# Performance work log

Measured on AMD Instinct MI355X. Metric: run time of the kernel, lower is better.

## Reference

```python
import jax, jax.numpy as jnp
import numpy as np

NMS_PRE, NMS_POST, NMS_THRESH = 1024, 512, 0.7
B, A, FEAT = 4, 70400, 27648
BN_EPS = 1e-5


def _bev_iou(boxes):
    # boxes: [K, 7] (x, y, z, dx, dy, dz, ry); axis-aligned BEV IoU
    x, y, dx, dy = boxes[:, 0], boxes[:, 1], boxes[:, 3], boxes[:, 4]
    x1, x2 = x - 0.5 * dx, x + 0.5 * dx
    y1, y2 = y - 0.5 * dy, y + 0.5 * dy
    iw = jnp.clip(jnp.minimum(x2[:, None], x2[None, :]) - jnp.maximum(x1[:, None], x1[None, :]), 0.0)
    ih = jnp.clip(jnp.minimum(y2[:, None], y2[None, :]) - jnp.maximum(y1[:, None], y1[None, :]), 0.0)
    inter = iw * ih
    area = dx * dy
    return inter / jnp.clip(area[:, None] + area[None, :] - inter, 1e-6)


def _greedy_nms(boxes, thresh):
    # boxes sorted by score desc; returns keep mask [K]
    K = boxes.shape[0]
    iou = _bev_iou(boxes)
    idx = jnp.arange(K)

    def step(keep, i):
        sup = (iou[i] > thresh) & (idx > i) & keep[i]
        return keep & ~sup, None

    keep, _ = jax.lax.scan(step, jnp.ones(K, dtype=bool), jnp.arange(K))
    return keep


def _proposal_one(box, cls):
    # box: [A, 7], cls: [A, n_cls]  ->  padded rois [NPOST,7], scores [NPOST], labels [NPOST]
    score = jnp.max(cls, axis=-1)
    label = jnp.argmax(cls, axis=-1)
    top_score, top_idx = jax.lax.top_k(score, NMS_PRE)
    top_box = box[top_idx]
    keep = _greedy_nms(top_box, NMS_THRESH)
    # stable: kept entries first, preserving score order
    order = jnp.argsort(jnp.where(keep, jnp.arange(NMS_PRE), NMS_PRE + jnp.arange(NMS_PRE)))
    sel = order[:NMS_POST]
    valid = jnp.arange(NMS_POST) < jnp.minimum(jnp.sum(keep), NMS_POST)
    rois = jnp.where(valid[:, None], top_box[sel], 0.0)
    roi_score = jnp.where(valid, top_score[sel], 0.0)
    roi_label = jnp.where(valid, label[top_idx][sel], 0) + 1  # +1 as in module
    return rois, roi_score, roi_label


def _bn_relu(h, g, b):
    # eval-mode BN with running_mean=0, running_var=1
    return jax.nn.relu(h * (g / jnp.sqrt(1.0 + BN_EPS)) + b)


def _decode(reg, anchors):
    # ResidualCoder_v1.decode_torch
    xa, ya, za = anchors[..., 0], anchors[..., 1], anchors[..., 2]
    dxa, dya, dza, ra = anchors[..., 3], anchors[..., 4], anchors[..., 5], anchors[..., 6]
    xt, yt, zt = reg[..., 0], reg[..., 1], reg[..., 2]
    dxt, dyt, dzt, rt = reg[..., 3], reg[..., 4], reg[..., 5], reg[..., 6]
    diag = jnp.sqrt(dxa * dxa + dya * dya)
    return jnp.stack([
        xt * diag + xa, yt * diag + ya, zt * dza + za,
        jnp.exp(dxt) * dxa, jnp.exp(dyt) * dya, jnp.exp(dzt) * dza,
        rt + ra], axis=-1)


def _rotate_z(box, ang):
    # rotate x,y of box [..., 7] by ang [...]
    c, s = jnp.cos(ang), jnp.sin(ang)
    x = box[..., 0] * c - box[..., 1] * s
    y = box[..., 0] * s + box[..., 1] * c
    return jnp.concatenate([x[..., None], y[..., None], box[..., 2:]], axis=-1)


def reference(rpn_box_preds, rpn_cls_preds, pooled_features,
              Ws1, g1, b1, Ws2, g2, b2,
              Wc1, gc1, bc1, Wc2, gc2, bc2, Wc3, bc3,
              Wr1, gr1, br1, Wr2, gr2, br2, Wr3, br3):
    # proposal_layer: per-batch topk + NMS + padded scatter (vmapped)
    rois, roi_scores, roi_labels = jax.vmap(_proposal_one)(rpn_box_preds, rpn_cls_preds)

    # shared / cls / reg heads (1x1 Conv1d == per-roi MLP), dropout off (eval)
    x = _bn_relu(pooled_features @ Ws1.T, g1, b1)
    x = _bn_relu(x @ Ws2.T, g2, b2)
    c = _bn_relu(x @ Wc1.T, gc1, bc1)
    c = _bn_relu(c @ Wc2.T, gc2, bc2)
    cls_preds = c @ Wc3.T + bc3          # [B*NPOST, 1]
    r = _bn_relu(x @ Wr1.T, gr1, br1)
    r = _bn_relu(r @ Wr2.T, gr2, br2)
    reg_preds = r @ Wr3.T + br3          # [B*NPOST, 7]

    bsz = rois.shape[0]
    cls_preds = cls_preds.reshape(bsz, -1, cls_preds.shape[-1])
    reg_preds = reg_preds.reshape(bsz, -1, 7)

    # generate_predict_box: decode against detached rois with xyz zeroed
    anchors = jax.lax.stop_gradient(rois)
    anchors = anchors.at[..., 0:3].set(0.0)
    box_ct = _decode(reg_preds, anchors)
    box_preds = _rotate_z(box_ct, rois[..., 6])
    box_preds = jnp.concatenate([box_preds[..., 0:3] + rois[..., 0:3], box_preds[..., 3:]], axis=-1)

    return jnp.concatenate([cls_preds, box_preds, roi_scores[..., None]], axis=-1)  # [B, NPOST, 9]


def setup_inputs():
    key = jax.random.key(0)
    ks = jax.random.split(key, 32)
    u = jax.random.uniform(ks[0], (B, A, 7), dtype=jnp.float32)
    lo = jnp.array([0.0, -40.0, -2.0, 1.5, 1.4, 1.0, -3.14159], jnp.float32)
    hi = jnp.array([70.0, 40.0, 0.0, 4.5, 2.0, 2.0, 3.14159], jnp.float32)
    rpn_box_preds = lo + u * (hi - lo)
    rpn_cls_preds = jax.random.normal(ks[1], (B, A, 3), dtype=jnp.float32)
    pooled_features = jax.random.normal(ks[2], (B * NMS_POST, FEAT), dtype=jnp.float32) * 0.1

    def w(k, o, i, std=None):
        s = (1.0 / np.sqrt(i)) if std is None else std
        return jax.random.normal(k, (o, i), dtype=jnp.float32) * s

    d = dict(
        rpn_box_preds=rpn_box_preds, rpn_cls_preds=rpn_cls_preds, pooled_features=pooled_features,
        Ws1=w(ks[3], 256, FEAT), g1=jnp.ones(256), b1=jnp.zeros(256),
        Ws2=w(ks[4], 256, 256), g2=jnp.ones(256), b2=jnp.zeros(256),
        Wc1=w(ks[5], 256, 256), gc1=jnp.ones(256), bc1=jnp.zeros(256),
        Wc2=w(ks[6], 256, 256), gc2=jnp.ones(256), bc2=jnp.zeros(256),
        Wc3=w(ks[7], 1, 256), bc3=jnp.zeros(1),
        Wr1=w(ks[8], 256, 256), gr1=jnp.ones(256), br1=jnp.zeros(256),
        Wr2=w(ks[9], 256, 256), gr2=jnp.ones(256), br2=jnp.zeros(256),
        Wr3=w(ks[10], 7, 256, std=0.001), br3=jnp.zeros(7),
    )
    return d
```

## Files before the change

### kernel.cpp

```cpp
#include <hip/hip_runtime.h>
#include <cstdint>

typedef unsigned int u32;
typedef unsigned long long u64;
typedef unsigned short u16;

#define BATCH 4
#define A_CNT 70400
#define FEAT 27648
#define KSPLIT 12
#define KCHUNK 2304
#define NTILE_IT 36

typedef __attribute__((ext_vector_type(8))) short bf16x8;
typedef __attribute__((ext_vector_type(4))) float f32x4;
typedef __attribute__((ext_vector_type(2))) u32 u32x2;
typedef __attribute__((ext_vector_type(4))) u32 u32x4;

constexpr size_t OF_KEYS = 0;
constexpr size_t OF_TBOX = OF_KEYS + 1126400;
constexpr size_t OF_TSC  = OF_TBOX + 114688;
constexpr size_t OF_BX1  = OF_TSC + 16384;
constexpr size_t OF_BX2  = OF_BX1 + 16384;
constexpr size_t OF_BY1  = OF_BX2 + 16384;
constexpr size_t OF_BY2  = OF_BY1 + 16384;
constexpr size_t OF_BAR  = OF_BY2 + 16384;
constexpr size_t OF_MASK = OF_BAR + 16384;
constexpr size_t OF_ROIS = OF_MASK + 524288;
constexpr size_t OF_RSC  = OF_ROIS + 57344;
constexpr size_t OF_BSW  = OF_RSC + 8192;
constexpr size_t OF_PART = OF_BSW + 14155776;
constexpr size_t WS_NEED = OF_PART + 33554432;

__device__ __forceinline__ u32 keyOf(float f) {
  u32 u = __float_as_uint(f);
  return (u & 0x80000000u) ? ~u : (u | 0x80000000u);
}
__device__ __forceinline__ float keyToF(u32 k) {
  u32 u = (k & 0x80000000u) ? (k ^ 0x80000000u) : ~k;
  return __uint_as_float(u);
}
__device__ __forceinline__ u16 f2bf(float f) {
  u32 u = __float_as_uint(f);
  u32 r = 0x7FFFu + ((u >> 16) & 1u);
  return (u16)((u + r) >> 16);
}
__device__ __forceinline__ void gload_lds16(const void* g, void* l) {
  auto gp = reinterpret_cast<const __attribute__((address_space(1))) unsigned int*>(
      reinterpret_cast<uintptr_t>(g));
  auto lp = reinterpret_cast<__attribute__((address_space(3))) unsigned int*>(
      reinterpret_cast<uintptr_t>(l));
  __builtin_amdgcn_global_load_lds(gp, lp, 16, 0, 0);
}
__device__ __forceinline__ u64 shflx64(u64 v, int m) {
  u32 lo = (u32)v, hi = (u32)(v >> 32);
  lo = __shfl_xor(lo, m, 64);
  hi = __shfl_xor(hi, m, 64);
  return ((u64)hi << 32) | lo;
}
__device__ __forceinline__ u32x4 pack8(float4 a, float4 b) {
  u32x4 o;
  o.x = (u32)f2bf(a.x) | ((u32)f2bf(a.y) << 16);
  o.y = (u32)f2bf(a.z) | ((u32)f2bf(a.w) << 16);
  o.z = (u32)f2bf(b.x) | ((u32)f2bf(b.y) << 16);
  o.w = (u32)f2bf(b.z) | ((u32)f2bf(b.w) << 16);
  return o;
}

__global__ __launch_bounds__(1024) void k_fatA(const float* __restrict__ cls,
    const float* __restrict__ Ws1, u32* __restrict__ keys, u32* __restrict__ Bsw)
{
  int bid = blockIdx.x;
  int t = threadIdx.x;
  if (bid < 864) {
    u32 w = (u32)bid * 1024u + t;
    u32 tile = w >> 11;
    u32 rem = w & 2047u;
    u32 n = rem >> 3;
    u32 pq = (rem & 7u) << 4;
    u32 q0 = pq ^ ((n & 7u) << 4);
    u32 col0 = tile * 64u + (q0 >> 1);
    const float* src = Ws1 + (size_t)n * FEAT + col0;
    float4 f0 = *(const float4*)src;
    float4 f1 = *(const float4*)(src + 4);
    ((u32x4*)Bsw)[w] = pack8(f0, f1);
    return;
  }
  u32 g = (u32)(bid - 864) * 1024u + t;
  float s0 = cls[(size_t)g * 3 + 0];
  float s1 = cls[(size_t)g * 3 + 1];
  float s2 = cls[(size_t)g * 3 + 2];
  keys[g] = keyOf(fmaxf(s0, fmaxf(s1, s2)));
}

__global__ __launch_bounds__(1024) void k_big(const u32* __restrict__ keys,
    const float* __restrict__ boxes, const float* __restrict__ A,
    const u32* __restrict__ Bsw, float* __restrict__ part,
    float* __restrict__ tbox, float* __restrict__ tsc,
    float* __restrict__ bx1, float* __restrict__ bx2, float* __restrict__ by1,
    float* __restrict__ by2, float* __restrict__ bar)
{
  __shared__ __align__(16) char smem[131072];
  int bid = blockIdx.x;
  int t = threadIdx.x;
  if (bid < 4) {
    int b = bid;
    int lane = t & 63, wv = t >> 6;
    const u32* kb = keys + (size_t)b * A_CNT;
    u64* s = (u64*)smem;
    u32* partials = (u32*)(smem + 16384);
    u32* ccp = (u32*)(smem + 16448);
    u32 h[35];
#pragma unroll
    for (int j = 0; j < 35; ++j) {
      int g0 = t + ((2 * j) << 10);
      int g1 = t + ((2 * j + 1) << 10);
      u32 a = (g0 < A_CNT) ? (kb[g0] >> 16) : 0u;
      u32 c2 = (g1 < A_CNT) ? (kb[g1] >> 16) : 0u;
      h[j] = a | (c2 << 16);
    }
    if (t == 0) ccp[0] = 0u;
    u32 lo = 0, hi = 65536;
    while (hi - lo > 1) {
      u32 mid = (lo + hi) >> 1;
      u32 c = 0;
#pragma unroll
      for (int j = 0; j < 35; ++j) {
        c += ((h[j] & 0xFFFFu) >= mid) ? 1u : 0u;
        c += ((h[j] >> 16) >= mid) ? 1u : 0u;
      }
#pragma unroll
      for (int o = 32; o > 0; o >>= 1) c += __shfl_xor(c, o, 64);
      __syncthreads();
      if (lane == 0) partials[wv] = c;
      __syncthreads();
      u32 tot = 0;
#pragma unroll
      for (int w2 = 0; w2 < 16; ++w2) tot += partials[w2];
      if (tot >= 1024u) lo = mid; else hi = mid;
    }
    u32 kth = lo;
    __syncthreads();
    u32 kc = kb[t];
#pragma unroll 1
    for (int i = 0; i < 69; ++i) {
      int g = t + (i << 10);
      u32 k = kc;
      if (i < 68) {
        int gn = t + ((i + 1) << 10);
        kc = (gn < A_CNT) ? kb[gn] : 0u;
      }
      bool pass = (g < A_CNT) && ((k >> 16) >= kth);
      u64 mm = __ballot(pass);
      if (mm) {
        int leader = __ffsll((unsigned long long)mm) - 1;
        u32 base = 0;
        if (lane == leader) base = atomicAdd(ccp, (u32)__popcll(mm));
        base = __shfl(base, leader, 64);
        if (pass) {
          u32 pos = base + (u32)__popcll(mm & ((1ull << lane) - 1ull));
          if (pos < 2048u) s[pos] = ((u64)k << 32) | (u32)(~(u32)g);
        }
      }
    }
    __syncthreads();
    u32 m = ccp[0]; if (m > 2048u) m = 2048u;
    for (int e = t; e < 2048; e += 1024) if (e >= (int)m) s[e] = 0ull;
    __syncthreads();
    {
      u64 v0 = s[2 * t], v1 = s[2 * t + 1];
#pragma unroll
      for (u32 k = 2; k <= 128; k <<= 1) {
        bool desc = ((t & (k >> 1)) == 0);
#pragma unroll
        for (u32 j = (k >> 1); j >= 2; j >>= 1) {
          u32 mmk = j >> 1;
          u64 p0 = shflx64(v0, mmk);
          u64 p1 = shflx64(v1, mmk);
          bool up = ((t & mmk) == 0);
          bool mx = (desc == up);
          v0 = mx ? (v0 > p0 ? v0 : p0) : (v0 < p0 ? v0 : p0);
          v1 = mx ? (v1 > p1 ? v1 : p1) : (v1 < p1 ? v1 : p1);
        }
        if (desc ? (v0 < v1) : (v0 > v1)) { u64 tmp = v0; v0 = v1; v1 = tmp; }
      }
      s[2 * t] = v0; s[2 * t + 1] = v1;
      __syncthreads();
      for (u32 k = 256; k <= 2048; k <<= 1) {
        for (u32 j = k >> 1; j >= 128; j >>= 1) {
          for (int e = t; e < 2048; e += 1024) {
            u32 p = (u32)e ^ j;
            if (p > (u32)e) {
              bool d2 = ((e & k) == 0);
              u64 x = s[e], y = s[p];
              if (d2 ? (x < y) : (x > y)) { s[e] = y; s[p] = x; }
            }
          }
          __syncthreads();
        }
        u64 v0 = s[2 * t], v1 = s[2 * t + 1];
        bool desc = ((t & (k >> 1)) == 0);
#pragma unroll
        for (u32 j = 64; j >= 2; j >>= 1) {
          u32 mmk = j >> 1;
          u64 p0 = shflx64(v0, mmk);
          u64 p1 = shflx64(v1, mmk);
          bool up = ((t & mmk) == 0);
          bool mx = (desc == up);
          v0 = mx ? (v0 > p0 ? v0 : p0) : (v0 < p0 ? v0 : p0);
          v1 = mx ? (v1 > p1 ? v1 : p1) : (v1 < p1 ? v1 : p1);
        }
        if (desc ? (v0 < v1) : (v0 > v1)) { u64 tmp = v0; v0 = v1; v1 = tmp; }
        s[2 * t] = v0; s[2 * t + 1] = v1;
        __syncthreads();
      }
    }
    u64 comp = s[t];
    u32 kk = (u32)(comp >> 32);
    u32 a = ~(u32)(comp & 0xFFFFFFFFull);
    int o = b * 1024 + t;
    tsc[o] = keyToF(kk);
    const float* bp = boxes + ((size_t)b * A_CNT + a) * 7;
    float x = bp[0], y = bp[1], z = bp[2], dx = bp[3], dy = bp[4], dz = bp[5], rr = bp[6];
    float* tb = tbox + (size_t)o * 7;
    tb[0] = x; tb[1] = y; tb[2] = z; tb[3] = dx; tb[4] = dy; tb[5] = dz; tb[6] = rr;
    {
#pragma clang fp contract(off)
      bx1[o] = x - 0.5f * dx; bx2[o] = x + 0.5f * dx;
      by1[o] = y - 0.5f * dy; by2[o] = y + 0.5f * dy;
      bar[o] = dx * dy;
    }
    return;
  }
  int bid2 = bid - 4;
  int ks = bid2 >> 4;
  int mt = bid2 & 15;
  int lane = t & 63, wvid = t >> 6;
  int row16 = lane & 15, kgrp = lane >> 4;
  int gm = wvid >> 2, gn = wvid & 3;

  f32x4 acc[2][4];
#pragma unroll
  for (int i = 0; i < 2; ++i)
#pragma unroll
    for (int j = 0; j < 4; ++j) acc[i][j] = (f32x4){0.f, 0.f, 0.f, 0.f};

  int arow = t >> 3;
  const float* ap_base = A + ((size_t)(mt * 128 + arow)) * FEAT + (size_t)ks * KCHUNK + (t & 7) * 8;
  int asw = (arow & 7) << 4;
  int awoff = arow * 128 + (((t & 7) * 16) ^ asw);
  const char* bsrc_base = (const char*)Bsw + ((size_t)(ks * NTILE_IT)) * 32768 + wvid * 2048 + lane * 16;
  int bdoff = wvid * 2048 + lane * 16;
  char* Abase = smem;
  char* Bbase = smem + 32768;

  int aoff[2][2], boff[4][2];
#pragma unroll
  for (int ksub = 0; ksub < 2; ++ksub) {
    int qq = ksub * 64 + kgrp * 16;
#pragma unroll
    for (int mf = 0; mf < 2; ++mf) {
      int row = gm * 32 + mf * 16 + row16;
      aoff[mf][ksub] = row * 128 + (qq ^ ((row & 7) << 4));
    }
#pragma unroll
    for (int nf = 0; nf < 4; ++nf) {
      int n = gn * 64 + nf * 16 + row16;
      boff[nf][ksub] = n * 128 + (qq ^ ((n & 7) << 4));
    }
  }

  float4 gaold0, gaold1;
  {
    const float4* ap0 = (const float4*)ap_base;
    float4 a00 = ap0[0], a01 = ap0[1];
    gload_lds16(bsrc_base, Bbase + bdoff);
    gload_lds16(bsrc_base + 1024, Bbase + bdoff + 1024);
    const float4* ap1 = (const float4*)(ap_base + 64);
    gaold0 = ap1[0]; gaold1 = ap1[1];
    const char* bs1 = bsrc_base + 32768;
    gload_lds16(bs1, Bbase + 32768 + bdoff);
    gload_lds16(bs1 + 1024, Bbase + 32768 + bdoff + 1024);
    *(u32x4*)(Abase + awoff) = pack8(a00, a01);
    asm volatile("s_waitcnt lgkmcnt(0)" ::: "memory");
    asm volatile("s_waitcnt vmcnt(4)" ::: "memory");
    __builtin_amdgcn_sched_barrier(0);
    __builtin_amdgcn_s_barrier();
  }

#pragma unroll 1
  for (int it = 0; it < NTILE_IT; ++it) {
    char* Acur = Abase + ((it & 1) << 14);
    char* Bcur = Bbase + (it % 3) * 32768;
    bool pf = (it + 2 < NTILE_IT);
    float4 gn0, gn1;
    if (pf) {
      const float4* ap = (const float4*)(ap_base + (it + 2) * 64);
      gn0 = ap[0]; gn1 = ap[1];
      const char* bs = bsrc_base + (size_t)(it + 2) * 32768;
      char* Bn = Bbase + ((it + 2) % 3) * 32768;
      gload_lds16(bs, Bn + bdoff);
      gload_lds16(bs + 1024, Bn + bdoff + 1024);
    }
    bf16x8 af[2][2], bf[4][2];
#pragma unroll
    for (int ksub = 0; ksub < 2; ++ksub) {
#pragma unroll
      for (int mf = 0; mf < 2; ++mf) af[mf][ksub] = *(const bf16x8*)(Acur + aoff[mf][ksub]);
#pragma unroll
      for (int nf = 0; nf < 4; ++nf) bf[nf][ksub] = *(const bf16x8*)(Bcur + boff[nf][ksub]);
    }
#pragma unroll
    for (int ksub = 0; ksub < 2; ++ksub)
#pragma unroll
      for (int mf = 0; mf < 2; ++mf)
#pragma unroll
        for (int nf = 0; nf < 4; ++nf)
          acc[mf][nf] = __builtin_amdgcn_mfma_f32_16x16x32_bf16(af[mf][ksub], bf[nf][ksub], acc[mf][nf], 0, 0, 0);
    if (it + 1 < NTILE_IT) {
      char* An = Abase + (((it + 1) & 1) << 14);
      *(u32x4*)(An + awoff) = pack8(gaold0, gaold1);
      gaold0 = gn0; gaold1 = gn1;
      asm volatile("s_waitcnt lgkmcnt(0)" ::: "memory");
      if (pf) asm volatile("s_waitcnt vmcnt(4)" ::: "memory");
      else    asm volatile("s_waitcnt vmcnt(0)" ::: "memory");
      __builtin_amdgcn_sched_barrier(0);
      __builtin_amdgcn_s_barrier();
    }
  }
  float* pb = part + (size_t)ks * 524288;
#pragma unroll
  for (int mf = 0; mf < 2; ++mf) {
    int orow = mt * 128 + gm * 32 + mf * 16 + kgrp * 4;
#pragma unroll
    for (int nf = 0; nf < 4; ++nf) {
      int col = gn * 64 + nf * 16 + row16;
#pragma unroll
      for (int rr = 0; rr < 4; ++rr)
        pb[(size_t)(orow + rr) * 256 + col] = acc[mf][nf][rr];
    }
  }
}

__global__ __launch_bounds__(1024) void k_mask(const float* __restrict__ bx1,
    const float* __restrict__ bx2, const float* __restrict__ by1,
    const float* __restrict__ by2, const float* __restrict__ bar,
    u32* __restrict__ mask)
{
  __shared__ float csm[16][5][64];
  int tt = threadIdx.x;
  int ug = tt >> 6, ln = tt & 63;
  int unit = blockIdx.x * 16 + ug;
  int b = unit >> 8, cbk = (unit >> 4) & 15, rb = unit & 15;
  int o = b * 1024, jc0 = cbk * 64;
  int r = rb * 64 + ln;
  csm[ug][0][ln] = bx1[o + jc0 + ln];
  csm[ug][1][ln] = bx2[o + jc0 + ln];
  csm[ug][2][ln] = by1[o + jc0 + ln];
  csm[ug][3][ln] = by2[o + jc0 + ln];
  csm[ug][4][ln] = bar[o + jc0 + ln];
  __syncthreads();
  float rx1 = bx1[o + r], rx2 = bx2[o + r], ry1 = by1[o + r], ry2 = by2[o + r], rar = bar[o + r];
  u32 w0 = 0, w1 = 0;
  {
#pragma clang fp contract(off)
    for (int c = 0; c < 64; ++c) {
      int jc = jc0 + c;
      float iw = fminf(rx2, csm[ug][1][c]) - fmaxf(rx1, csm[ug][0][c]); iw = fmaxf(iw, 0.0f);
      float ih = fminf(ry2, csm[ug][3][c]) - fmaxf(ry1, csm[ug][2][c]); ih = fmaxf(ih, 0.0f);
      float inter = iw * ih;
      float den = fmaxf(rar + csm[ug][4][c] - inter, 1e-6f);
      float iou = inter / den;
      if ((iou > 0.7f) && (jc > r)) {
        if (c < 32) w0 |= 1u << c; else w1 |= 1u << (c - 32);
      }
    }
  }
  mask[((size_t)(o + r)) * 32 + cbk * 2 + 0] = w0;
  mask[((size_t)(o + r)) * 32 + cbk * 2 + 1] = w1;
}

#define CHUNK_STEP(CUR, NXT, C) do {                                            \
    if ((C) + 1 < 32) {                                                         \
      int nb = ((C) + 1) * 1024 + el;                                           \
      _Pragma("unroll")                                                         \
      for (int i = 0; i < 32; ++i) NXT[i] = M[(size_t)(nb + i * 32)];           \
    }                                                                           \
    u32 w = R;                                                                  \
    _Pragma("unroll")                                                           \
    for (int i = 0; i < 32; ++i) w |= ((w >> i) & 1u) ? 0u : CUR[i];            \
    u32 wfin = __shfl(w, (C), 64);                                              \
    u32 m0 = 0, m1 = 0, m2 = 0, m3 = 0;                                         \
    _Pragma("unroll")                                                           \
    for (int i = 0; i < 32; i += 4) {                                           \
      m0 |= ((wfin >> (i + 0)) & 1u) ? 0u : CUR[i + 0];                         \
      m1 |= ((wfin >> (i + 1)) & 1u) ? 0u : CUR[i + 1];                         \
      m2 |= ((wfin >> (i + 2)) & 1u) ? 0u : CUR[i + 2];                         \
      m3 |= ((wfin >> (i + 3)) & 1u) ? 0u : CUR[i + 3];                         \
    }                                                                           \
    R |= (m0 | m1) | (m2 | m3);                                                 \
  } while (0)

__global__ __launch_bounds__(64) void k_nms(const u32* __restrict__ mask,
    const float* __restrict__ tbox, const float* __restrict__ tsc,
    float* __restrict__ rois, float* __restrict__ rsc)
{
  int b = blockIdx.x;
  int lane = threadIdx.x;
  int el = lane & 31;
  const u32* M = mask + (size_t)b * 1024 * 32;
  u32 R = 0;
  u32 bufA[32], bufB[32];
#pragma unroll
  for (int i = 0; i < 32; ++i) bufA[i] = M[(size_t)(i * 32 + el)];
#pragma unroll 1
  for (int c = 0; c < 32; c += 2) {
    CHUNK_STEP(bufA, bufB, c);
    CHUNK_STEP(bufB, bufA, c + 1);
  }
  u32 keepw = (lane < 32) ? ~R : 0u;
  int c = __popc(keepw);
  int pre = c;
  for (int d = 1; d < 64; d <<= 1) {
    int v = __shfl_up(pre, d, 64);
    if (lane >= d) pre += v;
  }
  int total = __shfl(pre, 31, 64);
  int base = pre - c;
  if (lane < 32) {
    u32 w = keepw;
    int rank = base;
    while (w) {
      int bit = __ffs(w) - 1;
      w &= w - 1;
      if (rank < 512) {
        int r = lane * 32 + bit;
        const float* tb = tbox + ((size_t)b * 1024 + r) * 7;
        float* rp = rois + ((size_t)b * 512 + rank) * 7;
        rp[0] = tb[0]; rp[1] = tb[1]; rp[2] = tb[2]; rp[3] = tb[3];
        rp[4] = tb[4]; rp[5] = tb[5]; rp[6] = tb[6];
        rsc[b * 512 + rank] = tsc[b * 1024 + r];
      }
      rank++;
    }
  }
  for (int z = total + lane; z < 512; z += 64) {
    float* rp = rois + ((size_t)b * 512 + z) * 7;
    rp[0] = rp[1] = rp[2] = rp[3] = rp[4] = rp[5] = rp[6] = 0.0f;
    rsc[b * 512 + z] = 0.0f;
  }
}

__device__ __forceinline__ void layer4(const float (*IN)[256], const float* __restrict__ W,
    const float* __restrict__ g, const float* __restrict__ bb, float (*OUT)[256], int t, int h)
{
  float acc[4] = {0, 0, 0, 0};
  const float* Wrow = W + (size_t)t * 256;
  for (int k = 0; k < 256; k += 4) {
    float4 w4 = *(const float4*)&Wrow[k];
#pragma unroll
    for (int r = 0; r < 4; ++r) {
      float4 xv = *(const float4*)&IN[h * 4 + r][k];
      acc[r] = fmaf(xv.x, w4.x, acc[r]);
      acc[r] = fmaf(xv.y, w4.y, acc[r]);
      acc[r] = fmaf(xv.z, w4.z, acc[r]);
      acc[r] = fmaf(xv.w, w4.w, acc[r]);
    }
  }
  float sc = g[t] / sqrtf(1.0f + 1e-5f);
  float bv = bb[t];
#pragma unroll
  for (int r = 0; r < 4; ++r)
    OUT[h * 4 + r][t] = fmaxf(fmaf(acc[r], sc, bv), 0.0f);
}

__global__ __launch_bounds__(512) void k_chain(const float* __restrict__ part,
    const float* __restrict__ Ws2, const float* __restrict__ Wc1, const float* __restrict__ Wc2,
    const float* __restrict__ Wr1, const float* __restrict__ Wr2,
    const float* __restrict__ g1, const float* __restrict__ b1,
    const float* __restrict__ g2, const float* __restrict__ b2,
    const float* __restrict__ gc1, const float* __restrict__ bc1,
    const float* __restrict__ gc2, const float* __restrict__ bc2,
    const float* __restrict__ gr1, const float* __restrict__ br1,
    const float* __restrict__ gr2, const float* __restrict__ br2,
    const float* __restrict__ Wc3, const float* __restrict__ bc3,
    const float* __restrict__ Wr3, const float* __restrict__ br3,
    const float* __restrict__ rois, const float* __restrict__ rsc,
    float* __restrict__ out)
{
  int bid = blockIdx.x, tid = threadIdx.x;
  int t = tid & 255, h = tid >> 8;
  __shared__ __align__(16) float bufX[8][256];
  __shared__ __align__(16) float bufY[8][256];
  __shared__ __align__(16) float bufC[8][256];
  __shared__ __align__(16) float bufR[8][256];
  __shared__ float hd[64];
  {
    float sc = g1[t] / sqrtf(1.0f + 1e-5f);
    float bv = b1[t];
#pragma unroll
    for (int r = 0; r < 4; ++r) {
      int row = h * 4 + r;
      float s = 0.f;
#pragma unroll
      for (int ks = 0; ks < KSPLIT; ++ks)
        s += part[(size_t)ks * 524288 + (size_t)(bid * 8 + row) * 256 + t];
      bufX[row][t] = fmaxf(fmaf(s, sc, bv), 0.0f);
    }
  }
  __syncthreads();
  layer4(bufX, Ws2, g2, b2, bufY, t, h);
  __syncthreads();
  layer4(bufY, Wc1, gc1, bc1, bufC, t, h);
  layer4(bufY, Wr1, gr1, br1, bufR, t, h);
  __syncthreads();
  layer4(bufC, Wc2, gc2, bc2, bufX, t, h);
  layer4(bufR, Wr2, gr2, br2, bufY, t, h);
  __syncthreads();
  int wv = tid >> 6, ln = tid & 63;
  for (int task = wv; task < 64; task += 8) {
    float p;
    if (task < 8) {
      float4 yv = *(const float4*)&bufX[task][ln * 4];
      float4 w4 = ((const float4*)Wc3)[ln];
      p = yv.x * w4.x + yv.y * w4.y + yv.z * w4.z + yv.w * w4.w;
    } else {
      int i = task - 8, row = i / 7, j = i % 7;
      float4 yv = *(const float4*)&bufY[row][ln * 4];
      float4 w4 = ((const float4*)(Wr3 + j * 256))[ln];
      p = yv.x * w4.x + yv.y * w4.y + yv.z * w4.z + yv.w * w4.w;
    }
#pragma unroll
    for (int off = 32; off > 0; off >>= 1) p += __shfl_xor(p, off, 64);
    if (ln == 0) hd[task] = p;
  }
  __syncthreads();
  if (tid < 8) {
    int m = bid * 8 + tid;
    float clsv = hd[tid] + bc3[0];
    float rg[7];
#pragma unroll
    for (int j = 0; j < 7; ++j) rg[j] = hd[8 + tid * 7 + j] + br3[j];
    const float* R = rois + (size_t)m * 7;
    float rx = R[0], ry = R[1], rz = R[2], dxa = R[3], dya = R[4], dza = R[5], ra = R[6];
    float diag = sqrtf(dxa * dxa + dya * dya);
    float x = rg[0] * diag, y = rg[1] * diag, z = rg[2] * dza;
    float ex = expf(rg[3]) * dxa, ey = expf(rg[4]) * dya, ez = expf(rg[5]) * dza;
    float hr = rg[6] + ra;
    float cc = cosf(ra), sn = sinf(ra);
    float xr = x * cc - y * sn, yr = x * sn + y * cc;
    float* O = out + (size_t)m * 9;
    O[0] = clsv; O[1] = xr + rx; O[2] = yr + ry; O[3] = z + rz;
    O[4] = ex; O[5] = ey; O[6] = ez; O[7] = hr; O[8] = rsc[m];
  }
}

extern "C" void kernel_launch(void* const* d_in, const int* in_sizes, int n_in,
                              void* d_out, int out_size, void* d_ws, size_t ws_size,
                              hipStream_t stream)
{
  const float* rpn_box = (const float*)d_in[0];
  const float* rpn_cls = (const float*)d_in[1];
  const float* pooled  = (const float*)d_in[2];
  const float* Ws1 = (const float*)d_in[3];
  const float* g1  = (const float*)d_in[4];
  const float* b1  = (const float*)d_in[5];
  const float* Ws2 = (const float*)d_in[6];
  const float* g2  = (const float*)d_in[7];
  const float* b2  = (const float*)d_in[8];
  const float* Wc1 = (const float*)d_in[9];
  const float* gc1 = (const float*)d_in[10];
  const float* bc1 = (const float*)d_in[11];
  const float* Wc2 = (const float*)d_in[12];
  const float* gc2 = (const float*)d_in[13];
  const float* bc2 = (const float*)d_in[14];
  const float* Wc3 = (const float*)d_in[15];
  const float* bc3 = (const float*)d_in[16];
  const float* Wr1 = (const float*)d_in[17];
  const float* gr1 = (const float*)d_in[18];
  const float* br1 = (const float*)d_in[19];
  const float* Wr2 = (const float*)d_in[20];
  const float* gr2 = (const float*)d_in[21];
  const float* br2 = (const float*)d_in[22];
  const float* Wr3 = (const float*)d_in[23];
  const float* br3 = (const float*)d_in[24];

  if (ws_size < WS_NEED) return;

  char* ws = (char*)d_ws;
  u32* keys = (u32*)(ws + OF_KEYS);
  float* tbox = (float*)(ws + OF_TBOX);
  float* tsc  = (float*)(ws + OF_TSC);
  float* bx1 = (float*)(ws + OF_BX1);
  float* bx2 = (float*)(ws + OF_BX2);
  float* by1 = (float*)(ws + OF_BY1);
  float* by2 = (float*)(ws + OF_BY2);
  float* bar = (float*)(ws + OF_BAR);
  u32* mask = (u32*)(ws + OF_MASK);
  float* roisb = (float*)(ws + OF_ROIS);
  float* rscb  = (float*)(ws + OF_RSC);
  u32* Bsw = (u32*)(ws + OF_BSW);
  float* part = (float*)(ws + OF_PART);

  k_fatA<<<1139, 1024, 0, stream>>>(rpn_cls, Ws1, keys, Bsw);
  k_big<<<196, 1024, 0, stream>>>(keys, rpn_box, pooled, Bsw, part,
                                  tbox, tsc, bx1, bx2, by1, by2, bar);
  k_mask<<<64, 1024, 0, stream>>>(bx1, bx2, by1, by2, bar, mask);
  k_nms<<<4, 64, 0, stream>>>(mask, tbox, tsc, roisb, rscb);
  k_chain<<<256, 512, 0, stream>>>(part, Ws2, Wc1, Wc2, Wr1, Wr2,
                                   g1, b1, g2, b2, gc1, bc1, gc2, bc2,
                                   gr1, br1, gr2, br2, Wc3, bc3, Wr3, br3,
                                   roisb, rscb, (float*)d_out);
}
```

Before: 216.6 us.

## Fuse IoU mask computation into NMS kernel using LDS-resident mask

Merges the separate IoU-mask kernel and the greedy NMS scan into one kernel per batch. Each of 1024 threads computes its row's suppression bits across all column blocks and stores them in a swizzled 128KB shared-memory mask. One wave then runs the serial scan from LDS instead of global memory. This removes a launch and a global mask round-trip, but cuts mask-compute parallelism from 64 blocks to 4 and drops the cross-chunk prefetch.

```diff
diff --git a/kernel.cpp b/kernel.cpp
--- a/kernel.cpp
+++ b/kernel.cpp
@@ -342,112 +342,95 @@
   }
 }
 
-__global__ __launch_bounds__(1024) void k_mask(const float* __restrict__ bx1,
+__global__ __launch_bounds__(1024) void k_nms(const float* __restrict__ bx1,
     const float* __restrict__ bx2, const float* __restrict__ by1,
     const float* __restrict__ by2, const float* __restrict__ bar,
-    u32* __restrict__ mask)
-{
-  __shared__ float csm[16][5][64];
-  int tt = threadIdx.x;
-  int ug = tt >> 6, ln = tt & 63;
-  int unit = blockIdx.x * 16 + ug;
-  int b = unit >> 8, cbk = (unit >> 4) & 15, rb = unit & 15;
-  int o = b * 1024, jc0 = cbk * 64;
-  int r = rb * 64 + ln;
-  csm[ug][0][ln] = bx1[o + jc0 + ln];
-  csm[ug][1][ln] = bx2[o + jc0 + ln];
-  csm[ug][2][ln] = by1[o + jc0 + ln];
-  csm[ug][3][ln] = by2[o + jc0 + ln];
-  csm[ug][4][ln] = bar[o + jc0 + ln];
-  __syncthreads();
-  float rx1 = bx1[o + r], rx2 = bx2[o + r], ry1 = by1[o + r], ry2 = by2[o + r], rar = bar[o + r];
-  u32 w0 = 0, w1 = 0;
-  {
-#pragma clang fp contract(off)
-    for (int c = 0; c < 64; ++c) {
-      int jc = jc0 + c;
-      float iw = fminf(rx2, csm[ug][1][c]) - fmaxf(rx1, csm[ug][0][c]); iw = fmaxf(iw, 0.0f);
-      float ih = fminf(ry2, csm[ug][3][c]) - fmaxf(ry1, csm[ug][2][c]); ih = fmaxf(ih, 0.0f);
-      float inter = iw * ih;
-      float den = fmaxf(rar + csm[ug][4][c] - inter, 1e-6f);
-      float iou = inter / den;
-      if ((iou > 0.7f) && (jc > r)) {
-        if (c < 32) w0 |= 1u << c; else w1 |= 1u << (c - 32);
-      }
-    }
-  }
-  mask[((size_t)(o + r)) * 32 + cbk * 2 + 0] = w0;
-  mask[((size_t)(o + r)) * 32 + cbk * 2 + 1] = w1;
-}
-
-#define CHUNK_STEP(CUR, NXT, C) do {                                            \
-    if ((C) + 1 < 32) {                                                         \
-      int nb = ((C) + 1) * 1024 + el;                                           \
-      _Pragma("unroll")                                                         \
-      for (int i = 0; i < 32; ++i) NXT[i] = M[(size_t)(nb + i * 32)];           \
-    }                                                                           \
-    u32 w = R;                                                                  \
-    _Pragma("unroll")                                                           \
-    for (int i = 0; i < 32; ++i) w |= ((w >> i) & 1u) ? 0u : CUR[i];            \
-    u32 wfin = __shfl(w, (C), 64);                                              \
-    u32 m0 = 0, m1 = 0, m2 = 0, m3 = 0;                                         \
-    _Pragma("unroll")                                                           \
-    for (int i = 0; i < 32; i += 4) {                                           \
-      m0 |= ((wfin >> (i + 0)) & 1u) ? 0u : CUR[i + 0];                         \
-      m1 |= ((wfin >> (i + 1)) & 1u) ? 0u : CUR[i + 1];                         \
-      m2 |= ((wfin >> (i + 2)) & 1u) ? 0u : CUR[i + 2];                         \
-      m3 |= ((wfin >> (i + 3)) & 1u) ? 0u : CUR[i + 3];                         \
-    }                                                                           \
-    R |= (m0 | m1) | (m2 | m3);                                                 \
-  } while (0)
-
-__global__ __launch_bounds__(64) void k_nms(const u32* __restrict__ mask,
     const float* __restrict__ tbox, const float* __restrict__ tsc,
     float* __restrict__ rois, float* __restrict__ rsc)
 {
-  int b = blockIdx.x;
-  int lane = threadIdx.x;
-  int el = lane & 31;
-  const u32* M = mask + (size_t)b * 1024 * 32;
-  u32 R = 0;
-  u32 bufA[32], bufB[32];
-#pragma unroll
-  for (int i = 0; i < 32; ++i) bufA[i] = M[(size_t)(i * 32 + el)];
+  __shared__ u32 Ml[1024 * 32];
+  int b = blockIdx.x, t = threadIdx.x;
+  int o = b * 1024;
+  float rx1 = bx1[o + t], rx2 = bx2[o + t], ry1 = by1[o + t], ry2 = by2[o + t], rar = bar[o + t];
 #pragma unroll 1
-  for (int c = 0; c < 32; c += 2) {
-    CHUNK_STEP(bufA, bufB, c);
-    CHUNK_STEP(bufB, bufA, c + 1);
-  }
-  u32 keepw = (lane < 32) ? ~R : 0u;
-  int c = __popc(keepw);
-  int pre = c;
-  for (int d = 1; d < 64; d <<= 1) {
-    int v = __shfl_up(pre, d, 64);
-    if (lane >= d) pre += v;
-  }
-  int total = __shfl(pre, 31, 64);
-  int base = pre - c;
-  if (lane < 32) {
-    u32 w = keepw;
-    int rank = base;
-    while (w) {
-      int bit = __ffs(w) - 1;
-      w &= w - 1;
-      if (rank < 512) {
-        int r = lane * 32 + bit;
-        const float* tb = tbox + ((size_t)b * 1024 + r) * 7;
-        float* rp = rois + ((size_t)b * 512 + rank) * 7;
-        rp[0] = tb[0]; rp[1] = tb[1]; rp[2] = tb[2]; rp[3] = tb[3];
-        rp[4] = tb[4]; rp[5] = tb[5]; rp[6] = tb[6];
-        rsc[b * 512 + rank] = tsc[b * 1024 + r];
-      }
-      rank++;
-    }
-  }
-  for (int z = total + lane; z < 512; z += 64) {
-    float* rp = rois + ((size_t)b * 512 + z) * 7;
-    rp[0] = rp[1] = rp[2] = rp[3] = rp[4] = rp[5] = rp[6] = 0.0f;
-    rsc[b * 512 + z] = 0.0f;
+  for (int cbk = 0; cbk < 16; ++cbk) {
+    int jc0 = cbk * 64;
+    u32 w0 = 0, w1 = 0;
+    {
+#pragma clang fp contract(off)
+      for (int c = 0; c < 64; ++c) {
+        int jc = jc0 + c;
+        float iw = fminf(rx2, bx2[o + jc]) - fmaxf(rx1, bx1[o + jc]); iw = fmaxf(iw, 0.0f);
+        float ih = fminf(ry2, by2[o + jc]) - fmaxf(ry1, by1[o + jc]); ih = fmaxf(ih, 0.0f);
+        float inter = iw * ih;
+        float den = fmaxf(rar + bar[o + jc] - inter, 1e-6f);
+        float iou = inter / den;
+        if ((iou > 0.7f) && (jc > t)) {
+          if (c < 32) w0 |= 1u << c; else w1 |= 1u << (c - 32);
+        }
+      }
+    }
+    Ml[t * 32 + ((cbk * 2) ^ (t & 31))] = w0;
+    Ml[t * 32 + ((cbk * 2 + 1) ^ (t & 31))] = w1;
+  }
+  __syncthreads();
+  if (t < 64) {
+    int lane = t;
+    int el = lane & 31;
+    u32 R = 0;
+#pragma unroll 1
+    for (int c = 0; c < 32; ++c) {
+      u32 cur[32];
+#pragma unroll
+      for (int i = 0; i < 32; ++i) {
+        int row = c * 32 + i;
+        cur[i] = Ml[row * 32 + (el ^ (row & 31))];
+      }
+      u32 w = R;
+#pragma unroll
+      for (int i = 0; i < 32; ++i) w |= ((w >> i) & 1u) ? 0u : cur[i];
+      u32 wfin = __shfl(w, c, 64);
+      u32 m0 = 0, m1 = 0, m2 = 0, m3 = 0;
+#pragma unroll
+      for (int i = 0; i < 32; i += 4) {
+        m0 |= ((wfin >> (i + 0)) & 1u) ? 0u : cur[i + 0];
+        m1 |= ((wfin >> (i + 1)) & 1u) ? 0u : cur[i + 1];
+        m2 |= ((wfin >> (i + 2)) & 1u) ? 0u : cur[i + 2];
+        m3 |= ((wfin >> (i + 3)) & 1u) ? 0u : cur[i + 3];
+      }
+      R |= (m0 | m1) | (m2 | m3);
+    }
+    u32 keepw = (lane < 32) ? ~R : 0u;
+    int c = __popc(keepw);
+    int pre = c;
+    for (int d = 1; d < 64; d <<= 1) {
+      int v = __shfl_up(pre, d, 64);
+      if (lane >= d) pre += v;
+    }
+    int total = __shfl(pre, 31, 64);
+    int base = pre - c;
+    if (lane < 32) {
+      u32 w = keepw;
+      int rank = base;
+      while (w) {
+        int bit = __ffs(w) - 1;
+        w &= w - 1;
+        if (rank < 512) {
+          int r = lane * 32 + bit;
+          const float* tb = tbox + ((size_t)b * 1024 + r) * 7;
+          float* rp = rois + ((size_t)b * 512 + rank) * 7;
+          rp[0] = tb[0]; rp[1] = tb[1]; rp[2] = tb[2]; rp[3] = tb[3];
+          rp[4] = tb[4]; rp[5] = tb[5]; rp[6] = tb[6];
+          rsc[b * 512 + rank] = tsc[b * 1024 + r];
+        }
+        rank++;
+      }
+    }
+    for (int z = total + lane; z < 512; z += 64) {
+      float* rp = rois + ((size_t)b * 512 + z) * 7;
+      rp[0] = rp[1] = rp[2] = rp[3] = rp[4] = rp[5] = rp[6] = 0.0f;
+      rsc[b * 512 + z] = 0.0f;
+    }
   }
 }
 
@@ -596,7 +579,6 @@
   float* by1 = (float*)(ws + OF_BY1);
   float* by2 = (float*)(ws + OF_BY2);
   float* bar = (float*)(ws + OF_BAR);
-  u32* mask = (u32*)(ws + OF_MASK);
   float* roisb = (float*)(ws + OF_ROIS);
   float* rscb  = (float*)(ws + OF_RSC);
   u32* Bsw = (u32*)(ws + OF_BSW);
@@ -605,8 +587,7 @@
   k_fatA<<<1139, 1024, 0, stream>>>(rpn_cls, Ws1, keys, Bsw);
   k_big<<<196, 1024, 0, stream>>>(keys, rpn_box, pooled, Bsw, part,
                                   tbox, tsc, bx1, bx2, by1, by2, bar);
-  k_mask<<<64, 1024, 0, stream>>>(bx1, bx2, by1, by2, bar, mask);
-  k_nms<<<4, 64, 0, stream>>>(mask, tbox, tsc, roisb, rscb);
+  k_nms<<<4, 1024, 0, stream>>>(bx1, bx2, by1, by2, bar, tbox, tsc, roisb, rscb);
   k_chain<<<256, 512, 0, stream>>>(part, Ws2, Wc1, Wc2, Wr1, Wr2,
                                    g1, b1, g2, b2, gc1, bc1, gc2, bc2,
                                    gr1, br1, gr2, br2, Wc3, bc3, Wr3, br3,
```

After: 457.2 us. 111% more time.
